# Kernel optimization log

Hardware: AMD Instinct MI355X
Metric: run time of the kernel (lower is better)

The kernel has to match this reference:

```python
import jax, jax.numpy as jnp
import numpy as np

N, NA, LAYERS = 8, 4, 4
NTOT = N + NA
DIM = 2 ** NTOT
B = 1024

# Diagonal of the fixed CZ brick layer (CZ is diagonal, so one elementwise pass per layer).
# Qubit 0 is the most-significant bit of the state index (tensorcircuit convention).
def _cz_diag():
    idx = np.arange(DIM)
    bits = (idx[None, :] >> (NTOT - 1 - np.arange(NTOT)[:, None])) & 1  # [NTOT, DIM]
    par = np.zeros(DIM, dtype=np.int64)
    for i in range(NTOT // 2):
        par += bits[2 * i] * bits[2 * i + 1]
    for i in range((NTOT - 1) // 2):
        par += bits[2 * i + 1] * bits[2 * i + 2]
    return jnp.asarray(1.0 - 2.0 * (par % 2), dtype=jnp.complex64)

CZ_DIAG = _cz_diag()

def _apply_1q(state, U, q):
    # state: [B, DIM]; apply 2x2 unitary U on qubit q (batched over samples)
    l, r = 2 ** q, 2 ** (NTOT - q - 1)
    s = state.reshape(-1, l, 2, r)
    return jnp.einsum('ij,bljr->blir', U, s).reshape(-1, DIM)

def _back_circuit(state, params):
    # hardware-efficient ansatz: per layer RX,RY on every qubit, then CZ bricks
    for lay in range(LAYERS):
        off = 2 * NTOT * lay
        for q in range(NTOT):
            th = params[off + q] * 0.5
            c = jnp.cos(th).astype(jnp.complex64)
            ms = (-1j) * jnp.sin(th).astype(jnp.complex64)
            Rx = jnp.stack([jnp.stack([c, ms]), jnp.stack([ms, c])])
            state = _apply_1q(state, Rx, q)
            th = params[off + NTOT + q] * 0.5
            c, s = jnp.cos(th), jnp.sin(th)
            Ry = jnp.stack([jnp.stack([c, -s]), jnp.stack([s, c])]).astype(jnp.complex64)
            state = _apply_1q(state, Ry, q)
        state = state * CZ_DIAG
    return state

def setup_inputs() -> dict:
    key = jax.random.key(0)
    k1, k2, k3, k4 = jax.random.split(key, 4)
    return {
        'inputs_re': jax.random.normal(k1, (B, DIM), jnp.float32),
        'inputs_im': jax.random.normal(k2, (B, DIM), jnp.float32),
        'params': jax.random.normal(k3, (2 * NTOT * LAYERS,), jnp.float32),
        'u': jax.random.uniform(k4, (B,), jnp.float32),
    }

def reference(inputs_re, inputs_im, params, u):
    state = (inputs_re + 1j * inputs_im).astype(jnp.complex64)
    full = _back_circuit(state, params)                      # [B, 2^n_tot]
    s3 = full.reshape(B, 2 ** NA, 2 ** N)                    # [B, 2^na, 2^n]
    probs = jnp.sum(s3.real ** 2 + s3.imag ** 2, axis=2)     # ancilla outcome probs
    cdf = jnp.cumsum(probs, axis=1)
    thresh = u * cdf[:, -1]                                  # inverse-CDF multinomial
    m = jnp.argmax(cdf >= thresh[:, None], axis=1)           # [B] sampled outcome
    post = s3[jnp.arange(B), m]                              # [B, 2^n] collapsed state
    norm = jnp.sqrt(jnp.sum(post.real ** 2 + post.imag ** 2, axis=1, keepdims=True))
    post = post / norm
    return jnp.stack([post.real, post.imag], axis=-1)        # [B, 2^n, 2]
```

## Files before the change

### kernel.cpp

```cpp
#include <hip/hip_runtime.h>
#include <math.h>

#define NTOT   12
#define DIM    4096
#define LAYERS 4
#define NB     1024

__device__ __forceinline__ int PHYS(int i) {
    return i ^ ((i >> 5) & 15) ^ (((i >> 9) & 1) << 4);
}

template<int G>
__device__ __forceinline__ void gate2(float (&xr)[16], float (&xi)[16],
                                      float cc, float ss, float cs, float sc) {
#pragma unroll
    for (int p = 0; p < 8; ++p) {
        const int j0 = ((p >> G) << (G + 1)) | (p & ((1 << G) - 1));
        const int j1 = j0 | (1 << G);
        const float x0r = xr[j0], x0i = xi[j0];
        const float x1r = xr[j1], x1i = xi[j1];
        xr[j0] = cc * x0r - ss * x0i - cs * x1r + sc * x1i;
        xi[j0] = cc * x0i + ss * x0r - cs * x1i - sc * x1r;
        xr[j1] = cs * x0r + sc * x0i + cc * x1r + ss * x1i;
        xi[j1] = cs * x0i - sc * x0r + cc * x1i - ss * x1r;
    }
}

__global__ __launch_bounds__(256, 4) void qddpm_kernel(
    const float* __restrict__ in_re,
    const float* __restrict__ in_im,
    const float* __restrict__ params,
    const float* __restrict__ uu,
    float* __restrict__ out)
{
    __shared__ float S[2 * DIM];
    __shared__ float CC[48], SS[48], CS[48], SC[48];
    __shared__ float sprob[16];
    __shared__ int   ssel;
    __shared__ float srnorm;

    const int b = blockIdx.x;
    const int t = threadIdx.x;

    {
        const float4* re4 = (const float4*)(in_re + (size_t)b * DIM);
        const float4* im4 = (const float4*)(in_im + (size_t)b * DIM);
#pragma unroll
        for (int k = 0; k < 4; ++k) {
            const int g = k * 256 + t;
            const float4 vr = re4[g];
            const float4 vi = im4[g];
            const int i0 = g * 4;
            S[PHYS(i0 + 0)] = vr.x; S[PHYS(i0 + 1)] = vr.y;
            S[PHYS(i0 + 2)] = vr.z; S[PHYS(i0 + 3)] = vr.w;
            S[DIM + PHYS(i0 + 0)] = vi.x; S[DIM + PHYS(i0 + 1)] = vi.y;
            S[DIM + PHYS(i0 + 2)] = vi.z; S[DIM + PHYS(i0 + 3)] = vi.w;
        }
        if (t < 48) {
            const int lay = t / 12, q = t - lay * 12;
            float c1, s1, c2, s2;
            sincosf(params[lay * 24 + q] * 0.5f, &s1, &c1);
            sincosf(params[lay * 24 + 12 + q] * 0.5f, &s2, &c2);
            CC[t] = c1 * c2; SS[t] = s1 * s2;
            CS[t] = c1 * s2; SC[t] = s1 * c2;
        }
    }
    __syncthreads();

    const int u    = t ^ (t >> 5);
    const int hi   = t >> 4, lo = t & 15;
    const int basB = hi * 256 + lo;
    const int xmB  = (hi & 3) << 3;
    const int basC = (t * 16) ^ ((t & 32) >> 1);
    const int wC   = (t >> 1) & 15;

    int smask = 0;
#pragma unroll
    for (int j = 0; j < 16; ++j) {
        const int i = t * 16 + j;
        smask |= (__popc(i & (i >> 1) & 0x7FF) & 1) << j;
    }

    float xr[16], xi[16];
    float partial = 0.0f;

    for (int lay = 0; lay < LAYERS; ++lay) {
        const int gb = lay * 12;

#pragma unroll
        for (int j = 0; j < 16; ++j) {
            const int p = j * 256 + (u ^ ((j & 3) << 3));
            xr[j] = S[p]; xi[j] = S[DIM + p];
        }
        gate2<0>(xr, xi, CC[gb + 3], SS[gb + 3], CS[gb + 3], SC[gb + 3]);
        gate2<1>(xr, xi, CC[gb + 2], SS[gb + 2], CS[gb + 2], SC[gb + 2]);
        gate2<2>(xr, xi, CC[gb + 1], SS[gb + 1], CS[gb + 1], SC[gb + 1]);
        gate2<3>(xr, xi, CC[gb + 0], SS[gb + 0], CS[gb + 0], SC[gb + 0]);
#pragma unroll
        for (int j = 0; j < 16; ++j) {
            const int p = j * 256 + (u ^ ((j & 3) << 3));
            S[p] = xr[j]; S[DIM + p] = xi[j];
        }
        __syncthreads();

#pragma unroll
        for (int j = 0; j < 16; ++j) {
            const int p = ((basB + j * 16) ^ xmB) ^ (j >> 1);
            xr[j] = S[p]; xi[j] = S[DIM + p];
        }
        gate2<0>(xr, xi, CC[gb + 7], SS[gb + 7], CS[gb + 7], SC[gb + 7]);
        gate2<1>(xr, xi, CC[gb + 6], SS[gb + 6], CS[gb + 6], SC[gb + 6]);
        gate2<2>(xr, xi, CC[gb + 5], SS[gb + 5], CS[gb + 5], SC[gb + 5]);
        gate2<3>(xr, xi, CC[gb + 4], SS[gb + 4], CS[gb + 4], SC[gb + 4]);
#pragma unroll
        for (int j = 0; j < 16; ++j) {
            const int p = ((basB + j * 16) ^ xmB) ^ (j >> 1);
            S[p] = xr[j]; S[DIM + p] = xi[j];
        }
        __syncthreads();

#pragma unroll
        for (int j = 0; j < 16; ++j) {
            const int p = basC + (j ^ wC);
            xr[j] = S[p]; xi[j] = S[DIM + p];
        }
        gate2<0>(xr, xi, CC[gb + 11], SS[gb + 11], CS[gb + 11], SC[gb + 11]);
        gate2<1>(xr, xi, CC[gb + 10], SS[gb + 10], CS[gb + 10], SC[gb + 10]);
        gate2<2>(xr, xi, CC[gb +  9], SS[gb +  9], CS[gb +  9], SC[gb +  9]);
        gate2<3>(xr, xi, CC[gb +  8], SS[gb +  8], CS[gb +  8], SC[gb +  8]);
#pragma unroll
        for (int j = 0; j < 16; ++j) {
            if (smask & (1 << j)) { xr[j] = -xr[j]; xi[j] = -xi[j]; }
        }
#pragma unroll
        for (int j = 0; j < 16; ++j) {
            const int p = basC + (j ^ wC);
            S[p] = xr[j]; S[DIM + p] = xi[j];
        }
        if (lay == LAYERS - 1) {
#pragma unroll
            for (int j = 0; j < 16; ++j)
                partial += xr[j] * xr[j] + xi[j] * xi[j];
        }
        __syncthreads();
    }

#pragma unroll
    for (int o = 8; o > 0; o >>= 1)
        partial += __shfl_down(partial, o, 16);
    if ((t & 15) == 0) sprob[t >> 4] = partial;
    __syncthreads();

    if (t == 0) {
        float cdf[16];
        float acc = 0.0f;
#pragma unroll
        for (int i = 0; i < 16; ++i) { acc += sprob[i]; cdf[i] = acc; }
        const float thresh = uu[b] * acc;
        int m = 0;
        for (int i = 0; i < 16; ++i) { if (cdf[i] >= thresh) { m = i; break; } }
        ssel = m;
        srnorm = 1.0f / sqrtf(sprob[m]);
    }
    __syncthreads();

    {
        const int m = ssel;
        const float rn = srnorm;
        const int p = m * 256 + (u ^ ((m & 3) << 3));
        ((float2*)out)[(size_t)b * 256 + t] = make_float2(S[p] * rn, S[DIM + p] * rn);
    }
}

extern "C" void kernel_launch(void* const* d_in, const int* in_sizes, int n_in,
                              void* d_out, int out_size, void* d_ws, size_t ws_size,
                              hipStream_t stream) {
    const float* in_re  = (const float*)d_in[0];
    const float* in_im  = (const float*)d_in[1];
    const float* params = (const float*)d_in[2];
    const float* u      = (const float*)d_in[3];
    float* out = (float*)d_out;
    qddpm_kernel<<<NB, 256, 0, stream>>>(in_re, in_im, params, u, out);
}
```

Measured before the change: 117.6 us.

## Interleave complex amplitudes in shared memory and vectorize gates with packed float2

Shared-memory state changes from split real/imag arrays to interleaved float2 with a new XOR swizzle, so each amplitude is one 64-bit LDS access instead of two 32-bit ones. The gate math is rewritten on 2-wide vectors so the compiler can emit packed FP32 ops, the gate coefficients are packed into float4, and the layer loop is fully unrolled. The aim is fewer LDS instructions and fewer ALU instructions. The new swizzle may introduce bank conflicts for 64-bit accesses, and full unrolling raises code size and register pressure.

```diff
diff --git a/kernel.cpp b/kernel.cpp
--- a/kernel.cpp
+++ b/kernel.cpp
@@ -6,23 +6,20 @@
 #define LAYERS 4
 #define NB     1024
 
-__device__ __forceinline__ int PHYS(int i) {
-    return i ^ ((i >> 5) & 15) ^ (((i >> 9) & 1) << 4);
-}
+typedef float v2f __attribute__((ext_vector_type(2)));
+
+__device__ __forceinline__ v2f ixv(v2f x) { return (v2f){ -x.y, x.x }; }
 
 template<int G>
-__device__ __forceinline__ void gate2(float (&xr)[16], float (&xi)[16],
-                                      float cc, float ss, float cs, float sc) {
+__device__ __forceinline__ void gate2(v2f (&x)[16], float cc, float ss, float cs, float sc) {
 #pragma unroll
     for (int p = 0; p < 8; ++p) {
         const int j0 = ((p >> G) << (G + 1)) | (p & ((1 << G) - 1));
         const int j1 = j0 | (1 << G);
-        const float x0r = xr[j0], x0i = xi[j0];
-        const float x1r = xr[j1], x1i = xi[j1];
-        xr[j0] = cc * x0r - ss * x0i - cs * x1r + sc * x1i;
-        xi[j0] = cc * x0i + ss * x0r - cs * x1i - sc * x1r;
-        xr[j1] = cs * x0r + sc * x0i + cc * x1r + ss * x1i;
-        xi[j1] = cs * x0i - sc * x0r + cc * x1i - ss * x1r;
+        const v2f x0 = x[j0], x1 = x[j1];
+        const v2f ix0 = ixv(x0), ix1 = ixv(x1);
+        x[j0] = cc * x0 + ss * ix0 - cs * x1 - sc * ix1;
+        x[j1] = cs * x0 - sc * ix0 + cc * x1 - ss * ix1;
     }
 }
 
@@ -33,11 +30,11 @@
     const float* __restrict__ uu,
     float* __restrict__ out)
 {
-    __shared__ float S[2 * DIM];
-    __shared__ float CC[48], SS[48], CS[48], SC[48];
-    __shared__ float sprob[16];
-    __shared__ int   ssel;
-    __shared__ float srnorm;
+    __shared__ v2f    S[DIM];
+    __shared__ float4 gco[48];
+    __shared__ float  sprob[16];
+    __shared__ int    ssel;
+    __shared__ float  srnorm;
 
     const int b = blockIdx.x;
     const int t = threadIdx.x;
@@ -47,32 +44,29 @@
         const float4* im4 = (const float4*)(in_im + (size_t)b * DIM);
 #pragma unroll
         for (int k = 0; k < 4; ++k) {
-            const int g = k * 256 + t;
+            const int g  = k * 256 + t;
             const float4 vr = re4[g];
             const float4 vi = im4[g];
             const int i0 = g * 4;
-            S[PHYS(i0 + 0)] = vr.x; S[PHYS(i0 + 1)] = vr.y;
-            S[PHYS(i0 + 2)] = vr.z; S[PHYS(i0 + 3)] = vr.w;
-            S[DIM + PHYS(i0 + 0)] = vi.x; S[DIM + PHYS(i0 + 1)] = vi.y;
-            S[DIM + PHYS(i0 + 2)] = vi.z; S[DIM + PHYS(i0 + 3)] = vi.w;
+            const int pb = i0 ^ ((i0 >> 4) & 15);
+            S[pb ^ 0] = (v2f){vr.x, vi.x};
+            S[pb ^ 1] = (v2f){vr.y, vi.y};
+            S[pb ^ 2] = (v2f){vr.z, vi.z};
+            S[pb ^ 3] = (v2f){vr.w, vi.w};
         }
         if (t < 48) {
             const int lay = t / 12, q = t - lay * 12;
             float c1, s1, c2, s2;
             sincosf(params[lay * 24 + q] * 0.5f, &s1, &c1);
             sincosf(params[lay * 24 + 12 + q] * 0.5f, &s2, &c2);
-            CC[t] = c1 * c2; SS[t] = s1 * s2;
-            CS[t] = c1 * s2; SC[t] = s1 * c2;
+            gco[t] = make_float4(c1 * c2, s1 * s2, c1 * s2, s1 * c2);
         }
     }
     __syncthreads();
 
-    const int u    = t ^ (t >> 5);
-    const int hi   = t >> 4, lo = t & 15;
-    const int basB = hi * 256 + lo;
-    const int xmB  = (hi & 3) << 3;
-    const int basC = (t * 16) ^ ((t & 32) >> 1);
-    const int wC   = (t >> 1) & 15;
+    const int baseA = t ^ ((t >> 4) & 15);
+    const int hiB = t >> 4, loB = t & 15;
+    const int baseC = t * 16, mC = t & 15;
 
     int smask = 0;
 #pragma unroll
@@ -81,70 +75,56 @@
         smask |= (__popc(i & (i >> 1) & 0x7FF) & 1) << j;
     }
 
-    float xr[16], xi[16];
-    float partial = 0.0f;
+    v2f x[16];
+    v2f acc2 = (v2f){0.0f, 0.0f};
 
+#pragma unroll
     for (int lay = 0; lay < LAYERS; ++lay) {
         const int gb = lay * 12;
 
 #pragma unroll
-        for (int j = 0; j < 16; ++j) {
-            const int p = j * 256 + (u ^ ((j & 3) << 3));
-            xr[j] = S[p]; xi[j] = S[DIM + p];
-        }
-        gate2<0>(xr, xi, CC[gb + 3], SS[gb + 3], CS[gb + 3], SC[gb + 3]);
-        gate2<1>(xr, xi, CC[gb + 2], SS[gb + 2], CS[gb + 2], SC[gb + 2]);
-        gate2<2>(xr, xi, CC[gb + 1], SS[gb + 1], CS[gb + 1], SC[gb + 1]);
-        gate2<3>(xr, xi, CC[gb + 0], SS[gb + 0], CS[gb + 0], SC[gb + 0]);
+        for (int j = 0; j < 16; ++j) x[j] = S[j * 256 + baseA];
+        { float4 c;
+          c = gco[gb + 3]; gate2<0>(x, c.x, c.y, c.z, c.w);
+          c = gco[gb + 2]; gate2<1>(x, c.x, c.y, c.z, c.w);
+          c = gco[gb + 1]; gate2<2>(x, c.x, c.y, c.z, c.w);
+          c = gco[gb + 0]; gate2<3>(x, c.x, c.y, c.z, c.w); }
 #pragma unroll
-        for (int j = 0; j < 16; ++j) {
-            const int p = j * 256 + (u ^ ((j & 3) << 3));
-            S[p] = xr[j]; S[DIM + p] = xi[j];
-        }
+        for (int j = 0; j < 16; ++j) S[j * 256 + baseA] = x[j];
         __syncthreads();
 
 #pragma unroll
-        for (int j = 0; j < 16; ++j) {
-            const int p = ((basB + j * 16) ^ xmB) ^ (j >> 1);
-            xr[j] = S[p]; xi[j] = S[DIM + p];
-        }
-        gate2<0>(xr, xi, CC[gb + 7], SS[gb + 7], CS[gb + 7], SC[gb + 7]);
-        gate2<1>(xr, xi, CC[gb + 6], SS[gb + 6], CS[gb + 6], SC[gb + 6]);
-        gate2<2>(xr, xi, CC[gb + 5], SS[gb + 5], CS[gb + 5], SC[gb + 5]);
-        gate2<3>(xr, xi, CC[gb + 4], SS[gb + 4], CS[gb + 4], SC[gb + 4]);
+        for (int j = 0; j < 16; ++j) x[j] = S[hiB * 256 + j * 16 + (loB ^ j)];
+        { float4 c;
+          c = gco[gb + 7]; gate2<0>(x, c.x, c.y, c.z, c.w);
+          c = gco[gb + 6]; gate2<1>(x, c.x, c.y, c.z, c.w);
+          c = gco[gb + 5]; gate2<2>(x, c.x, c.y, c.z, c.w);
+          c = gco[gb + 4]; gate2<3>(x, c.x, c.y, c.z, c.w); }
 #pragma unroll
-        for (int j = 0; j < 16; ++j) {
-            const int p = ((basB + j * 16) ^ xmB) ^ (j >> 1);
-            S[p] = xr[j]; S[DIM + p] = xi[j];
-        }
+        for (int j = 0; j < 16; ++j) S[hiB * 256 + j * 16 + (loB ^ j)] = x[j];
         __syncthreads();
 
 #pragma unroll
-        for (int j = 0; j < 16; ++j) {
-            const int p = basC + (j ^ wC);
-            xr[j] = S[p]; xi[j] = S[DIM + p];
-        }
-        gate2<0>(xr, xi, CC[gb + 11], SS[gb + 11], CS[gb + 11], SC[gb + 11]);
-        gate2<1>(xr, xi, CC[gb + 10], SS[gb + 10], CS[gb + 10], SC[gb + 10]);
-        gate2<2>(xr, xi, CC[gb +  9], SS[gb +  9], CS[gb +  9], SC[gb +  9]);
-        gate2<3>(xr, xi, CC[gb +  8], SS[gb +  8], CS[gb +  8], SC[gb +  8]);
+        for (int j = 0; j < 16; ++j) x[j] = S[baseC + (j ^ mC)];
+        { float4 c;
+          c = gco[gb + 11]; gate2<0>(x, c.x, c.y, c.z, c.w);
+          c = gco[gb + 10]; gate2<1>(x, c.x, c.y, c.z, c.w);
+          c = gco[gb +  9]; gate2<2>(x, c.x, c.y, c.z, c.w);
+          c = gco[gb +  8]; gate2<3>(x, c.x, c.y, c.z, c.w); }
 #pragma unroll
         for (int j = 0; j < 16; ++j) {
-            if (smask & (1 << j)) { xr[j] = -xr[j]; xi[j] = -xi[j]; }
-        }
-#pragma unroll
-        for (int j = 0; j < 16; ++j) {
-            const int p = basC + (j ^ wC);
-            S[p] = xr[j]; S[DIM + p] = xi[j];
+            if (smask & (1 << j)) x[j] = -x[j];
         }
         if (lay == LAYERS - 1) {
 #pragma unroll
-            for (int j = 0; j < 16; ++j)
-                partial += xr[j] * xr[j] + xi[j] * xi[j];
+            for (int j = 0; j < 16; ++j) acc2 += x[j] * x[j];
         }
+#pragma unroll
+        for (int j = 0; j < 16; ++j) S[baseC + (j ^ mC)] = x[j];
         __syncthreads();
     }
 
+    float partial = acc2.x + acc2.y;
 #pragma unroll
     for (int o = 8; o > 0; o >>= 1)
         partial += __shfl_down(partial, o, 16);
@@ -153,10 +133,10 @@
 
     if (t == 0) {
         float cdf[16];
-        float acc = 0.0f;
+        float a = 0.0f;
 #pragma unroll
-        for (int i = 0; i < 16; ++i) { acc += sprob[i]; cdf[i] = acc; }
-        const float thresh = uu[b] * acc;
+        for (int i = 0; i < 16; ++i) { a += sprob[i]; cdf[i] = a; }
+        const float thresh = uu[b] * a;
         int m = 0;
         for (int i = 0; i < 16; ++i) { if (cdf[i] >= thresh) { m = i; break; } }
         ssel = m;
@@ -167,8 +147,8 @@
     {
         const int m = ssel;
         const float rn = srnorm;
-        const int p = m * 256 + (u ^ ((m & 3) << 3));
-        ((float2*)out)[(size_t)b * 256 + t] = make_float2(S[p] * rn, S[DIM + p] * rn);
+        const v2f a = S[m * 256 + baseA];
+        ((float2*)out)[(size_t)b * 256 + t] = make_float2(a.x * rn, a.y * rn);
     }
 }
 
```

Result: no change. 117.5 us (-0.0%).
